# Performance work log

Measured on AMD Instinct MI355X. Metric: run time of the kernel, lower is better.

The kernel has to match this reference:

```python
import jax, jax.numpy as jnp
import numpy as np

N, E, G = 50000, 800000, 1024
IN, HID, H, L = 128, 128, 4, 3
C = HID // H  # per-head channels = 32
NEG_SLOPE = 0.2
BN_EPS = 1e-5


def setup_inputs() -> dict:
    key = jax.random.key(0)
    ks = jax.random.split(key, 12)
    s = 0.05
    x = jax.random.normal(ks[0], (N, IN), dtype=jnp.float32)
    edge_index = jax.random.randint(ks[1], (2, E), 0, N, dtype=jnp.int32)
    batch = jnp.sort(jax.random.randint(ks[2], (N,), 0, G, dtype=jnp.int32))
    # GATConv params per layer (in_dim == hidden_dim so all layers stack)
    Ws = jax.random.normal(ks[3], (L, HID, HID), dtype=jnp.float32) * s
    att_src = jax.random.normal(ks[4], (L, H, C), dtype=jnp.float32) * s
    att_dst = jax.random.normal(ks[5], (L, H, C), dtype=jnp.float32) * s
    biases = jax.random.normal(ks[6], (L, HID), dtype=jnp.float32) * s
    gammas = jnp.ones((L, HID), dtype=jnp.float32)
    betas = jnp.zeros((L, HID), dtype=jnp.float32)
    lin1_w = jax.random.normal(ks[7], (HID, HID // 2), dtype=jnp.float32) * s
    lin1_b = jnp.zeros((HID // 2,), dtype=jnp.float32)
    lin2_w = jax.random.normal(ks[8], (HID // 2, 1), dtype=jnp.float32) * s
    lin2_b = jnp.zeros((1,), dtype=jnp.float32)
    return dict(x=x, edge_index=edge_index, batch=batch, Ws=Ws, att_src=att_src,
                att_dst=att_dst, biases=biases, gammas=gammas, betas=betas,
                lin1_w=lin1_w, lin1_b=lin1_b, lin2_w=lin2_w, lin2_b=lin2_b)


def _gat_layer(x, src, dst, W, a_src, a_dst, bias):
    h = (x @ W).reshape(N, H, C)                      # [N,H,C]
    e_src = jnp.einsum('nhc,hc->nh', h, a_src)        # [N,H]
    e_dst = jnp.einsum('nhc,hc->nh', h, a_dst)
    e = jax.nn.leaky_relu(e_src[src] + e_dst[dst], NEG_SLOPE)  # [E',H]
    m = jax.ops.segment_max(e, dst, num_segments=N)   # segment softmax over dst
    ex = jnp.exp(e - m[dst])
    den = jax.ops.segment_sum(ex, dst, num_segments=N)
    alpha = ex / (den[dst] + 1e-16)
    msg = h[src] * alpha[:, :, None]                  # [E',H,C]
    out = jax.ops.segment_sum(msg, dst, num_segments=N).reshape(N, HID)
    return out + bias


def reference(x, edge_index, batch, Ws, att_src, att_dst, biases, gammas, betas,
              lin1_w, lin1_b, lin2_w, lin2_b):
    loop = jnp.arange(N, dtype=edge_index.dtype)      # add_self_loops=True
    src = jnp.concatenate([edge_index[0], loop])
    dst = jnp.concatenate([edge_index[1], loop])
    for l in range(L):
        h = _gat_layer(x, src, dst, Ws[l], att_src[l], att_dst[l], biases[l])
        mean = h.mean(axis=0)                         # BatchNorm1d (batch stats)
        var = h.var(axis=0)
        h = (h - mean) / jnp.sqrt(var + BN_EPS) * gammas[l] + betas[l]
        x = jax.nn.elu(h)
    cnt = jax.ops.segment_sum(jnp.ones((N,), x.dtype), batch, num_segments=G)
    pooled = jax.ops.segment_sum(x, batch, num_segments=G) / jnp.maximum(cnt, 1.0)[:, None]
    h1 = jax.nn.relu(pooled @ lin1_w + lin1_b)
    return (h1 @ lin2_w + lin2_b)[:, 0]               # [G]
```

## Files before the change

### kernel.cpp

```cpp
#include <hip/hip_runtime.h>
#include <hip/hip_fp16.h>
#include <math.h>

#define NN 50000
#define EE 800000
#define GG 1024
#define HIDD 128
#define NHEAD 4
#define EPTOT (EE + NN)
#define NEG_SLOPE 0.2f
#define NB ((NN + 255) / 256)
#define NTILE (NN / 16)
#define LOG2E 1.4426950408889634f

#define BSHIFT 9
#define NBUK 98
#define PCHUNK 4096
#define BCAP 10240

typedef _Float16 f16x8 __attribute__((ext_vector_type(8)));
typedef float f32x4 __attribute__((ext_vector_type(4)));

__global__ void zero_kernel(float* __restrict__ p, int n) {
  int i = blockIdx.x * blockDim.x + threadIdx.x;
  if (i < n) p[i] = 0.f;
}

__global__ void count_kernel(const int* __restrict__ ei, int* __restrict__ deg) {
  int e = blockIdx.x * blockDim.x + threadIdx.x;
  if (e >= EPTOT) return;
  int d = (e < EE) ? ei[EE + e] : (e - EE);
  atomicAdd(&deg[d], 1);
}

__global__ __launch_bounds__(256) void degsum_kernel(const int* __restrict__ deg,
                                                     int* __restrict__ bsum) {
  __shared__ int sh[256];
  int i = blockIdx.x * 256 + threadIdx.x;
  sh[threadIdx.x] = (i < NN) ? deg[i] : 0;
  __syncthreads();
  for (int off = 128; off > 0; off >>= 1) {
    if (threadIdx.x < off) sh[threadIdx.x] += sh[threadIdx.x + off];
    __syncthreads();
  }
  if (threadIdx.x == 0) bsum[blockIdx.x] = sh[0];
}

__global__ __launch_bounds__(256) void scanb_kernel(const int* __restrict__ bsum,
                                                    int* __restrict__ boff,
                                                    int* __restrict__ rowptr,
                                                    int* __restrict__ bcur) {
  __shared__ int sh[256];
  int t = threadIdx.x;
  int v = (t < NB) ? bsum[t] : 0;
  sh[t] = v;
  __syncthreads();
  for (int off = 1; off < 256; off <<= 1) {
    int u = (t >= off) ? sh[t - off] : 0;
    __syncthreads();
    sh[t] += u;
    __syncthreads();
  }
  if (t < NB) boff[t] = sh[t] - v;
  if (!(t & 1) && (t >> 1) < NBUK) bcur[t >> 1] = sh[t] - v;
  if (t == 255) rowptr[NN] = sh[255];
}

__global__ __launch_bounds__(256) void rowptr_kernel(const int* __restrict__ deg,
                                                     const int* __restrict__ boff,
                                                     int* __restrict__ rowptr) {
  __shared__ int sh[256];
  int t = threadIdx.x;
  int i = blockIdx.x * 256 + t;
  int v = (i < NN) ? deg[i] : 0;
  sh[t] = v;
  __syncthreads();
  for (int off = 1; off < 256; off <<= 1) {
    int u = (t >= off) ? sh[t - off] : 0;
    __syncthreads();
    sh[t] += u;
    __syncthreads();
  }
  if (i < NN) rowptr[i] = boff[blockIdx.x] + sh[t] - v;
}

__global__ __launch_bounds__(256) void partA_kernel(const int* __restrict__ ei,
                                                    int* __restrict__ bcur,
                                                    unsigned long long* __restrict__ pairs) {
  __shared__ int hist[NBUK];
  __shared__ int sbase[NBUK];
  int t = threadIdx.x;
  if (t < NBUK) hist[t] = 0;
  __syncthreads();
  int e0 = blockIdx.x * PCHUNK;
  int ss[16], dd[16];
  int cnt = 0;
#pragma unroll
  for (int i = 0; i < 16; ++i) {
    int e = e0 + i * 256 + t;
    if (e < EPTOT) {
      int s, d;
      if (e < EE) { s = ei[e]; d = ei[EE + e]; } else { s = e - EE; d = s; }
      ss[cnt] = s; dd[cnt] = d; ++cnt;
      atomicAdd(&hist[d >> BSHIFT], 1);
    }
  }
  __syncthreads();
  if (t < NBUK) {
    int h = hist[t];
    sbase[t] = h ? atomicAdd(&bcur[t], h) : 0;
    hist[t] = 0;
  }
  __syncthreads();
  for (int i = 0; i < cnt; ++i) {
    int b = dd[i] >> BSHIFT;
    int pos = sbase[b] + atomicAdd(&hist[b], 1);
    pairs[pos] = ((unsigned long long)(unsigned)dd[i] << 32) | (unsigned)ss[i];
  }
}

__global__ __launch_bounds__(512) void partB_kernel(const unsigned long long* __restrict__ pairs,
                                                    const int* __restrict__ rowptr,
                                                    int* __restrict__ colb) {
  __shared__ int cur[512];
  __shared__ int stage[BCAP];
  int b = blockIdx.x;
  int t = threadIdx.x;
  int node0 = b << BSHIFT;
  int node1 = min(node0 + 512, NN);
  int base = rowptr[node0];
  int nE = rowptr[node1] - base;
  cur[t] = (node0 + t < node1) ? (rowptr[node0 + t] - base) : 0;
  __syncthreads();
  for (int j = t; j < nE; j += 512) {
    unsigned long long p = pairs[base + j];
    int d = (int)(p >> 32);
    int s = (int)(p & 0xffffffffu);
    int pl = atomicAdd(&cur[d - node0], 1);
    if (pl < BCAP) stage[pl] = s;
    else colb[base + pl] = s;
  }
  __syncthreads();
  int lim = min(nE, BCAP);
  for (int j = t; j < lim; j += 512) colb[base + j] = stage[j];
}

__device__ inline float bnelu1(float v, float scale, float shift) {
  v = v * scale + shift;
  return (v > 0.f) ? v : expm1f(v);
}

__global__ __launch_bounds__(256) void prepack_kernel(const float* __restrict__ Ws,
                                                      _Float16* __restrict__ Wp) {
  int f = blockIdx.x * 256 + threadIdx.x;
  if (f >= 3 * 2048) return;
  int layer = f >> 11, r = f & 2047;
  int ctile = r >> 8, ks = (r >> 6) & 3, lane = r & 63;
  const float* W = Ws + (size_t)layer * HIDD * HIDD;
  int col = ctile * 16 + (lane & 15);
  int krow = ks * 32 + (lane >> 4) * 8;
  f16x8 v;
#pragma unroll
  for (int j = 0; j < 8; ++j) v[j] = (_Float16)W[(krow + j) * HIDD + col];
  *(f16x8*)(Wp + f * 8) = v;
}

__global__ void bnfinal_kernel(const float* __restrict__ stat,
                               const float* __restrict__ gamma,
                               const float* __restrict__ beta,
                               float* __restrict__ scsh) {
  int c = threadIdx.x;
  const float invN = 1.f / (float)NN;
  float mean = stat[c] * invN;
  float var = stat[128 + c] * invN - mean * mean;
  float scale = gamma[c] * rsqrtf(var + 1e-5f);
  scsh[c] = scale;
  scsh[128 + c] = beta[c] - mean * scale;
}

__global__ __launch_bounds__(256) void gemm_mfma_kernel(
    const float* __restrict__ Xf, const __half* __restrict__ Xh,
    const _Float16* __restrict__ Wp, const float* __restrict__ scsh,
    const float* __restrict__ asrc, const float* __restrict__ adst,
    __half* __restrict__ Hh, float* __restrict__ esrc, float* __restrict__ edst) {
  int wave = threadIdx.x >> 6, lane = threadIdx.x & 63;
  int jt = blockIdx.x * 4 + wave;
  if (jt >= NTILE) return;
  int nl = lane & 15, kg = lane >> 4;
  int node = jt * 16 + nl;
  f32x4 acc[8];
#pragma unroll
  for (int c = 0; c < 8; ++c) acc[c] = (f32x4){0.f, 0.f, 0.f, 0.f};
#pragma unroll
  for (int ks = 0; ks < 4; ++ks) {
    int k0 = ks * 32 + kg * 8;
    f16x8 bfrag;
    if (Xf) {
      const float* xrow = Xf + node * HIDD;
      float4 va = *(const float4*)(xrow + k0);
      float4 vb = *(const float4*)(xrow + k0 + 4);
      bfrag[0] = (_Float16)va.x; bfrag[1] = (_Float16)va.y;
      bfrag[2] = (_Float16)va.z; bfrag[3] = (_Float16)va.w;
      bfrag[4] = (_Float16)vb.x; bfrag[5] = (_Float16)vb.y;
      bfrag[6] = (_Float16)vb.z; bfrag[7] = (_Float16)vb.w;
    } else {
      float4 raw = *(const float4*)(Xh + node * HIDD + k0);
      const __half2* hp = (const __half2*)&raw;
      float4 s0 = *(const float4*)(scsh + k0);
      float4 s1 = *(const float4*)(scsh + k0 + 4);
      float4 t0 = *(const float4*)(scsh + HIDD + k0);
      float4 t1 = *(const float4*)(scsh + HIDD + k0 + 4);
      float2 f0 = __half22float2(hp[0]);
      float2 f1 = __half22float2(hp[1]);
      float2 f2 = __half22float2(hp[2]);
      float2 f3 = __half22float2(hp[3]);
      bfrag[0] = (_Float16)bnelu1(f0.x, s0.x, t0.x);
      bfrag[1] = (_Float16)bnelu1(f0.y, s0.y, t0.y);
      bfrag[2] = (_Float16)bnelu1(f1.x, s0.z, t0.z);
      bfrag[3] = (_Float16)bnelu1(f1.y, s0.w, t0.w);
      bfrag[4] = (_Float16)bnelu1(f2.x, s1.x, t1.x);
      bfrag[5] = (_Float16)bnelu1(f2.y, s1.y, t1.y);
      bfrag[6] = (_Float16)bnelu1(f3.x, s1.z, t1.z);
      bfrag[7] = (_Float16)bnelu1(f3.y, s1.w, t1.w);
    }
#pragma unroll
    for (int c = 0; c < 8; ++c) {
      f16x8 afrag = *(const f16x8*)(Wp + (((c * 4 + ks) * 64 + lane) << 3));
      acc[c] = __builtin_amdgcn_mfma_f32_16x16x32_f16(afrag, bfrag, acc[c], 0, 0, 0);
    }
  }
  float es_p[4] = {0.f, 0.f, 0.f, 0.f};
  float ed_p[4] = {0.f, 0.f, 0.f, 0.f};
  __half* hrow = Hh + node * HIDD;
#pragma unroll
  for (int c = 0; c < 8; ++c) {
    int ch0 = c * 16 + kg * 4;
    __half2 h01 = __floats2half2_rn(acc[c][0], acc[c][1]);
    __half2 h23 = __floats2half2_rn(acc[c][2], acc[c][3]);
    union { __half2 h[2]; float2 f; } u;
    u.h[0] = h01; u.h[1] = h23;
    *(float2*)(hrow + ch0) = u.f;
    float4 av = *(const float4*)(asrc + ch0);
    float4 bv = *(const float4*)(adst + ch0);
    int hd = c >> 1;
    es_p[hd] += acc[c][0] * av.x + acc[c][1] * av.y + acc[c][2] * av.z + acc[c][3] * av.w;
    ed_p[hd] += acc[c][0] * bv.x + acc[c][1] * bv.y + acc[c][2] * bv.z + acc[c][3] * bv.w;
  }
#pragma unroll
  for (int hd = 0; hd < 4; ++hd) {
    es_p[hd] += __shfl_xor(es_p[hd], 16);
    es_p[hd] += __shfl_xor(es_p[hd], 32);
    ed_p[hd] += __shfl_xor(ed_p[hd], 16);
    ed_p[hd] += __shfl_xor(ed_p[hd], 32);
  }
  float es_o = (kg == 0) ? es_p[0] : (kg == 1) ? es_p[1] : (kg == 2) ? es_p[2] : es_p[3];
  float ed_o = (kg == 0) ? ed_p[0] : (kg == 1) ? ed_p[1] : (kg == 2) ? ed_p[2] : ed_p[3];
  esrc[node * 4 + kg] = es_o * LOG2E;
  edst[node * 4 + kg] = ed_o * LOG2E;
}

__global__ __launch_bounds__(256) void agg_kernel(const __half2* __restrict__ Hh,
                                                  const float* __restrict__ esrc,
                                                  const float* __restrict__ edst,
                                                  const int* __restrict__ rowptr,
                                                  const int* __restrict__ colb,
                                                  const float* __restrict__ bias,
                                                  __half* __restrict__ outh) {
  int lane = threadIdx.x & 63;
  int wid = __builtin_amdgcn_readfirstlane((int)((blockIdx.x * 256 + threadIdx.x) >> 6));
  int hd = lane >> 4;
  float ed = edst[wid * 4 + hd];
  int e0 = rowptr[wid];
  int deg = rowptr[wid + 1] - e0;
  float den = 0.f, ax = 0.f, ay = 0.f;
  for (int base = 0; base < deg; base += 64) {
    int rem = deg - base;
    if (rem > 64) rem = 64;
    int edg = 0;
    if (base + lane < deg) edg = colb[e0 + base + lane];
    int j = 0;
    for (; j + 8 <= rem; j += 8) {
      int sA = __builtin_amdgcn_readlane(edg, j + 0);
      int sB = __builtin_amdgcn_readlane(edg, j + 1);
      int sC = __builtin_amdgcn_readlane(edg, j + 2);
      int sD = __builtin_amdgcn_readlane(edg, j + 3);
      int sE = __builtin_amdgcn_readlane(edg, j + 4);
      int sF = __builtin_amdgcn_readlane(edg, j + 5);
      int sG = __builtin_amdgcn_readlane(edg, j + 6);
      int sH = __builtin_amdgcn_readlane(edg, j + 7);
      float eA = esrc[sA * 4 + hd]; __half2 hA = Hh[sA * 64 + lane];
      float eB = esrc[sB * 4 + hd]; __half2 hB = Hh[sB * 64 + lane];
      float eC = esrc[sC * 4 + hd]; __half2 hC = Hh[sC * 64 + lane];
      float eD = esrc[sD * 4 + hd]; __half2 hD = Hh[sD * 64 + lane];
      float eE = esrc[sE * 4 + hd]; __half2 hE = Hh[sE * 64 + lane];
      float eF = esrc[sF * 4 + hd]; __half2 hF = Hh[sF * 64 + lane];
      float eG = esrc[sG * 4 + hd]; __half2 hG = Hh[sG * 64 + lane];
      float eH = esrc[sH * 4 + hd]; __half2 hH = Hh[sH * 64 + lane];
#define EDGE_MATH(EV, HV)                          \
      {                                            \
        float z = (EV) + ed;                       \
        z = fmaxf(z, z * NEG_SLOPE);               \
        float w = exp2f(z);                        \
        float2 f = __half22float2(HV);             \
        den += w;                                  \
        ax = fmaf(w, f.x, ax);                     \
        ay = fmaf(w, f.y, ay);                     \
      }
      EDGE_MATH(eA, hA) EDGE_MATH(eB, hB) EDGE_MATH(eC, hC) EDGE_MATH(eD, hD)
      EDGE_MATH(eE, hE) EDGE_MATH(eF, hF) EDGE_MATH(eG, hG) EDGE_MATH(eH, hH)
    }
    for (; j < rem; ++j) {
      int sA = __builtin_amdgcn_readlane(edg, j);
      float eA = esrc[sA * 4 + hd];
      __half2 hA = Hh[sA * 64 + lane];
      EDGE_MATH(eA, hA)
    }
#undef EDGE_MATH
  }
  float inv = 1.f / (den + 1e-16f);
  int c = 2 * lane;
  float vx = ax * inv + bias[c];
  float vy = ay * inv + bias[c + 1];
  ((__half2*)outh)[wid * 64 + lane] = __floats2half2_rn(vx, vy);
}

__global__ __launch_bounds__(256) void bnstat_kernel(const __half* __restrict__ X,
                                                     float* __restrict__ stat) {
  __shared__ float sh[256];
  int tid = threadIdx.x;
  int c = tid & 127;
  int half = tid >> 7;
  float s = 0.f, q = 0.f;
  for (int r = blockIdx.x * 2 + half; r < NN; r += gridDim.x * 2) {
    float v = __half2float(X[r * HIDD + c]);
    s += v;
    q += v * v;
  }
  sh[tid] = s;
  __syncthreads();
  if (tid < 128) atomicAdd(&stat[c], s + sh[tid + 128]);
  __syncthreads();
  sh[tid] = q;
  __syncthreads();
  if (tid < 128) atomicAdd(&stat[128 + c], q + sh[tid + 128]);
}

__global__ void gbound_kernel(const int* __restrict__ batch, int* __restrict__ gstart) {
  int i = blockIdx.x * blockDim.x + threadIdx.x;
  if (i >= NN) return;
  int cur = batch[i];
  int prev = (i == 0) ? -1 : batch[i - 1];
  for (int g = prev + 1; g <= cur; ++g) gstart[g] = i;
  if (i == NN - 1) {
    for (int g = cur + 1; g <= GG; ++g) gstart[g] = NN;
  }
}

__global__ __launch_bounds__(128) void poolhead_kernel(const __half* __restrict__ X,
                                                       const int* __restrict__ gstart,
                                                       const float* __restrict__ scsh,
                                                       const float* __restrict__ w1,
                                                       const float* __restrict__ b1,
                                                       const float* __restrict__ w2,
                                                       const float* __restrict__ b2,
                                                       float* __restrict__ out) {
  __shared__ float pl[HIDD];
  int g = blockIdx.x;
  int c = threadIdx.x;
  float scale = scsh[c];
  float shift = scsh[128 + c];
  int n0 = gstart[g], n1 = gstart[g + 1];
  float s = 0.f;
  for (int n = n0; n < n1; ++n)
    s += bnelu1(__half2float(X[n * HIDD + c]), scale, shift);
  float inv = (n1 > n0) ? 1.f / (float)(n1 - n0) : 0.f;
  pl[c] = s * inv;
  __syncthreads();
  if (c < 64) {
    float acc = b1[c];
#pragma unroll 4
    for (int k = 0; k < HIDD; ++k) acc += pl[k] * w1[k * 64 + c];
    acc = fmaxf(acc, 0.f);
    float v = acc * w2[c];
#pragma unroll
    for (int off = 32; off > 0; off >>= 1) v += __shfl_down(v, off);
    if (c == 0) out[g] = v + b2[0];
  }
}

extern "C" void kernel_launch(void* const* d_in, const int* in_sizes, int n_in,
                              void* d_out, int out_size, void* d_ws, size_t ws_size,
                              hipStream_t stream) {
  const float* x    = (const float*)d_in[0];
  const int* ei     = (const int*)d_in[1];
  const int* batch  = (const int*)d_in[2];
  const float* Ws   = (const float*)d_in[3];
  const float* asrc = (const float*)d_in[4];
  const float* adst = (const float*)d_in[5];
  const float* bias = (const float*)d_in[6];
  const float* gam  = (const float*)d_in[7];
  const float* bet  = (const float*)d_in[8];
  const float* w1   = (const float*)d_in[9];
  const float* b1   = (const float*)d_in[10];
  const float* w2   = (const float*)d_in[11];
  const float* b2   = (const float*)d_in[12];
  float* out = (float*)d_out;

  char* wp = (char*)d_ws;
  auto carve = [&](size_t bytes) -> char* {
    char* p = wp;
    wp += (bytes + 255) & ~(size_t)255;
    return p;
  };
  __half* B     = (__half*)carve((size_t)NN * HIDD * 2);
  __half* Hh    = (__half*)carve((size_t)NN * HIDD * 2);
  _Float16* Wp  = (_Float16*)carve((size_t)3 * HIDD * HIDD * 2);
  float* scsh   = (float*)carve((size_t)3 * 256 * 4);
  float* esrc   = (float*)carve((size_t)NN * NHEAD * 4);
  float* edst   = (float*)carve((size_t)NN * NHEAD * 4);
  int* rowptr   = (int*)carve((size_t)(NN + 1) * 4);
  int* colb     = (int*)carve((size_t)EPTOT * 4);
  unsigned long long* pairs = (unsigned long long*)carve((size_t)EPTOT * 8);
  int* bcur     = (int*)carve((size_t)NBUK * 4);
  int* bsum     = (int*)carve((size_t)NB * 4);
  int* boff     = (int*)carve((size_t)NB * 4);
  int* gstart   = (int*)carve((size_t)(GG + 1) * 4);
  char* z0 = wp;
  int* deg      = (int*)carve((size_t)NN * 4);
  float* stats  = (float*)carve(768 * 4);
  int zcount = (int)((wp - z0) / 4);

  zero_kernel<<<(zcount + 255) / 256, 256, 0, stream>>>((float*)z0, zcount);
  prepack_kernel<<<24, 256, 0, stream>>>(Ws, Wp);
  count_kernel<<<(EPTOT + 255) / 256, 256, 0, stream>>>(ei, deg);
  degsum_kernel<<<NB, 256, 0, stream>>>(deg, bsum);
  scanb_kernel<<<1, 256, 0, stream>>>(bsum, boff, rowptr, bcur);
  rowptr_kernel<<<NB, 256, 0, stream>>>(deg, boff, rowptr);
  partA_kernel<<<(EPTOT + PCHUNK - 1) / PCHUNK, 256, 0, stream>>>(ei, bcur, pairs);
  partB_kernel<<<NBUK, 512, 0, stream>>>(pairs, rowptr, colb);
  gbound_kernel<<<(NN + 255) / 256, 256, 0, stream>>>(batch, gstart);

  for (int l = 0; l < 3; ++l) {
    const float* sc_prev = (l == 0) ? nullptr : scsh + (l - 1) * 256;
    const float* xf = (l == 0) ? x : nullptr;
    const __half* xh = (l == 0) ? nullptr : B;
    gemm_mfma_kernel<<<(NTILE + 3) / 4, 256, 0, stream>>>(
        xf, xh, Wp + (size_t)l * HIDD * HIDD, sc_prev,
        asrc + l * NHEAD * 32, adst + l * NHEAD * 32, Hh, esrc, edst);
    agg_kernel<<<(NN * 64 + 255) / 256, 256, 0, stream>>>(
        (const __half2*)Hh, esrc, edst, rowptr, colb, bias + l * HIDD, B);
    bnstat_kernel<<<1024, 256, 0, stream>>>(B, stats + l * 256);
    bnfinal_kernel<<<1, 128, 0, stream>>>(stats + l * 256, gam + l * HIDD,
                                          bet + l * HIDD, scsh + l * 256);
  }
  poolhead_kernel<<<GG, 128, 0, stream>>>(B, gstart, scsh + 2 * 256, w1, b1, w2, b2, out);
}
```

Before: 391.1 us.

## Store features in per-head slabs and aggregate one head per launch

```diff
diff --git a/kernel.cpp b/kernel.cpp
--- a/kernel.cpp
+++ b/kernel.cpp
@@ -12,6 +12,7 @@
 #define NB ((NN + 255) / 256)
 #define NTILE (NN / 16)
 #define LOG2E 1.4426950408889634f
+#define HSLAB (NN * 32)
 
 #define BSHIFT 9
 #define NBUK 98
@@ -204,7 +205,7 @@
       bfrag[4] = (_Float16)vb.x; bfrag[5] = (_Float16)vb.y;
       bfrag[6] = (_Float16)vb.z; bfrag[7] = (_Float16)vb.w;
     } else {
-      float4 raw = *(const float4*)(Xh + node * HIDD + k0);
+      float4 raw = *(const float4*)(Xh + ks * HSLAB + node * 32 + kg * 8);
       const __half2* hp = (const __half2*)&raw;
       float4 s0 = *(const float4*)(scsh + k0);
       float4 s1 = *(const float4*)(scsh + k0 + 4);
@@ -231,18 +232,18 @@
   }
   float es_p[4] = {0.f, 0.f, 0.f, 0.f};
   float ed_p[4] = {0.f, 0.f, 0.f, 0.f};
-  __half* hrow = Hh + node * HIDD;
 #pragma unroll
   for (int c = 0; c < 8; ++c) {
     int ch0 = c * 16 + kg * 4;
+    int hd = c >> 1;
+    int chin = (c & 1) * 16 + kg * 4;
     __half2 h01 = __floats2half2_rn(acc[c][0], acc[c][1]);
     __half2 h23 = __floats2half2_rn(acc[c][2], acc[c][3]);
     union { __half2 h[2]; float2 f; } u;
     u.h[0] = h01; u.h[1] = h23;
-    *(float2*)(hrow + ch0) = u.f;
+    *(float2*)(Hh + hd * HSLAB + node * 32 + chin) = u.f;
     float4 av = *(const float4*)(asrc + ch0);
     float4 bv = *(const float4*)(adst + ch0);
-    int hd = c >> 1;
     es_p[hd] += acc[c][0] * av.x + acc[c][1] * av.y + acc[c][2] * av.z + acc[c][3] * av.w;
     ed_p[hd] += acc[c][0] * bv.x + acc[c][1] * bv.y + acc[c][2] * bv.z + acc[c][3] * bv.w;
   }
@@ -255,21 +256,22 @@
   }
   float es_o = (kg == 0) ? es_p[0] : (kg == 1) ? es_p[1] : (kg == 2) ? es_p[2] : es_p[3];
   float ed_o = (kg == 0) ? ed_p[0] : (kg == 1) ? ed_p[1] : (kg == 2) ? ed_p[2] : ed_p[3];
-  esrc[node * 4 + kg] = es_o * LOG2E;
-  edst[node * 4 + kg] = ed_o * LOG2E;
-}
-
-__global__ __launch_bounds__(256) void agg_kernel(const __half2* __restrict__ Hh,
-                                                  const float* __restrict__ esrc,
-                                                  const float* __restrict__ edst,
-                                                  const int* __restrict__ rowptr,
-                                                  const int* __restrict__ colb,
-                                                  const float* __restrict__ bias,
-                                                  __half* __restrict__ outh) {
+  esrc[kg * NN + node] = es_o * LOG2E;
+  edst[kg * NN + node] = ed_o * LOG2E;
+}
+
+__global__ __launch_bounds__(256) void aggh_kernel(const __half* __restrict__ HhH,
+                                                   const float* __restrict__ esrcH,
+                                                   const float* __restrict__ edstH,
+                                                   const int* __restrict__ rowptr,
+                                                   const int* __restrict__ colb,
+                                                   const float* __restrict__ biasH,
+                                                   __half* __restrict__ outH) {
   int lane = threadIdx.x & 63;
-  int wid = __builtin_amdgcn_readfirstlane((int)((blockIdx.x * 256 + threadIdx.x) >> 6));
-  int hd = lane >> 4;
-  float ed = edst[wid * 4 + hd];
+  int wid = (blockIdx.x * 256 + threadIdx.x) >> 6;
+  int qw = lane >> 4;
+  int cl = lane & 15;
+  float ed = edstH[wid];
   int e0 = rowptr[wid];
   int deg = rowptr[wid + 1] - e0;
   float den = 0.f, ax = 0.f, ay = 0.f;
@@ -278,50 +280,31 @@
     if (rem > 64) rem = 64;
     int edg = 0;
     if (base + lane < deg) edg = colb[e0 + base + lane];
-    int j = 0;
-    for (; j + 8 <= rem; j += 8) {
-      int sA = __builtin_amdgcn_readlane(edg, j + 0);
-      int sB = __builtin_amdgcn_readlane(edg, j + 1);
-      int sC = __builtin_amdgcn_readlane(edg, j + 2);
-      int sD = __builtin_amdgcn_readlane(edg, j + 3);
-      int sE = __builtin_amdgcn_readlane(edg, j + 4);
-      int sF = __builtin_amdgcn_readlane(edg, j + 5);
-      int sG = __builtin_amdgcn_readlane(edg, j + 6);
-      int sH = __builtin_amdgcn_readlane(edg, j + 7);
-      float eA = esrc[sA * 4 + hd]; __half2 hA = Hh[sA * 64 + lane];
-      float eB = esrc[sB * 4 + hd]; __half2 hB = Hh[sB * 64 + lane];
-      float eC = esrc[sC * 4 + hd]; __half2 hC = Hh[sC * 64 + lane];
-      float eD = esrc[sD * 4 + hd]; __half2 hD = Hh[sD * 64 + lane];
-      float eE = esrc[sE * 4 + hd]; __half2 hE = Hh[sE * 64 + lane];
-      float eF = esrc[sF * 4 + hd]; __half2 hF = Hh[sF * 64 + lane];
-      float eG = esrc[sG * 4 + hd]; __half2 hG = Hh[sG * 64 + lane];
-      float eH = esrc[sH * 4 + hd]; __half2 hH = Hh[sH * 64 + lane];
-#define EDGE_MATH(EV, HV)                          \
-      {                                            \
-        float z = (EV) + ed;                       \
-        z = fmaxf(z, z * NEG_SLOPE);               \
-        float w = exp2f(z);                        \
-        float2 f = __half22float2(HV);             \
-        den += w;                                  \
-        ax = fmaf(w, f.x, ax);                     \
-        ay = fmaf(w, f.y, ay);                     \
-      }
-      EDGE_MATH(eA, hA) EDGE_MATH(eB, hB) EDGE_MATH(eC, hC) EDGE_MATH(eD, hD)
-      EDGE_MATH(eE, hE) EDGE_MATH(eF, hF) EDGE_MATH(eG, hG) EDGE_MATH(eH, hH)
+    int iters = (rem + 3) >> 2;
+    for (int i = 0; i < iters; ++i) {
+      int slot = i * 4 + qw;
+      int s = __shfl(edg, slot);
+      float es = esrcH[s];
+      __half2 hv = *(const __half2*)(HhH + s * 32 + cl * 2);
+      float z = es + ed;
+      z = fmaxf(z, z * NEG_SLOPE);
+      float w = exp2f(z);
+      w = (base + slot < deg) ? w : 0.f;
+      float2 f = __half22float2(hv);
+      den += w;
+      ax = fmaf(w, f.x, ax);
+      ay = fmaf(w, f.y, ay);
     }
-    for (; j < rem; ++j) {
-      int sA = __builtin_amdgcn_readlane(edg, j);
-      float eA = esrc[sA * 4 + hd];
-      __half2 hA = Hh[sA * 64 + lane];
-      EDGE_MATH(eA, hA)
-    }
-#undef EDGE_MATH
-  }
-  float inv = 1.f / (den + 1e-16f);
-  int c = 2 * lane;
-  float vx = ax * inv + bias[c];
-  float vy = ay * inv + bias[c + 1];
-  ((__half2*)outh)[wid * 64 + lane] = __floats2half2_rn(vx, vy);
+  }
+  den += __shfl_xor(den, 16); den += __shfl_xor(den, 32);
+  ax  += __shfl_xor(ax, 16);  ax  += __shfl_xor(ax, 32);
+  ay  += __shfl_xor(ay, 16);  ay  += __shfl_xor(ay, 32);
+  if (lane < 16) {
+    float inv = 1.f / (den + 1e-16f);
+    float vx = ax * inv + biasH[2 * cl];
+    float vy = ay * inv + biasH[2 * cl + 1];
+    ((__half2*)outH)[wid * 16 + cl] = __floats2half2_rn(vx, vy);
+  }
 }
 
 __global__ __launch_bounds__(256) void bnstat_kernel(const __half* __restrict__ X,
@@ -330,9 +313,10 @@
   int tid = threadIdx.x;
   int c = tid & 127;
   int half = tid >> 7;
+  const __half* Xs = X + (c >> 5) * HSLAB + (c & 31);
   float s = 0.f, q = 0.f;
   for (int r = blockIdx.x * 2 + half; r < NN; r += gridDim.x * 2) {
-    float v = __half2float(X[r * HIDD + c]);
+    float v = __half2float(Xs[r * 32]);
     s += v;
     q += v * v;
   }
@@ -369,10 +353,11 @@
   int c = threadIdx.x;
   float scale = scsh[c];
   float shift = scsh[128 + c];
+  const __half* Xs = X + (c >> 5) * HSLAB + (c & 31);
   int n0 = gstart[g], n1 = gstart[g + 1];
   float s = 0.f;
   for (int n = n0; n < n1; ++n)
-    s += bnelu1(__half2float(X[n * HIDD + c]), scale, shift);
+    s += bnelu1(__half2float(Xs[n * 32]), scale, shift);
   float inv = (n1 > n0) ? 1.f / (float)(n1 - n0) : 0.f;
   pl[c] = s * inv;
   __syncthreads();
@@ -447,8 +432,11 @@
     gemm_mfma_kernel<<<(NTILE + 3) / 4, 256, 0, stream>>>(
         xf, xh, Wp + (size_t)l * HIDD * HIDD, sc_prev,
         asrc + l * NHEAD * 32, adst + l * NHEAD * 32, Hh, esrc, edst);
-    agg_kernel<<<(NN * 64 + 255) / 256, 256, 0, stream>>>(
-        (const __half2*)Hh, esrc, edst, rowptr, colb, bias + l * HIDD, B);
+    for (int h = 0; h < NHEAD; ++h) {
+      aggh_kernel<<<NN / 4, 256, 0, stream>>>(
+          Hh + h * HSLAB, esrc + h * NN, edst + h * NN, rowptr, colb,
+          bias + l * HIDD + h * 32, B + h * HSLAB);
+    }
     bnstat_kernel<<<1024, 256, 0, stream>>>(B, stats + l * 256);
     bnfinal_kernel<<<1, 128, 0, stream>>>(stats + l * 256, gam + l * HIDD,
                                           bet + l * HIDD, scsh + l * 256);
```

Measured after the change: 568.3 us. 45.3% more time.
